# Kernel optimization log

Hardware: AMD Instinct MI355X
Metric: run time of the kernel (lower is better)

The kernel has to match this reference:

```python
import jax, jax.numpy as jnp
import numpy as np

B, LP, LQ, H = 16, 2048, 2048, 1024

def setup_inputs() -> dict:
    key = jax.random.key(0)
    k1, k2, k3 = jax.random.split(key, 3)
    proj_p = jax.random.normal(k1, (B, LP, H), dtype=jnp.float32)
    proj_q = jax.random.normal(k2, (B, LQ, H), dtype=jnp.float32)
    # nn.Linear(hidden_size, hidden_size): W stored as [out, in], y = x @ W.T + b
    W = jax.random.normal(k3, (H, H), dtype=jnp.float32) * (1.0 / np.sqrt(H))
    b = jnp.zeros((H,), dtype=jnp.float32)
    return {"proj_p": proj_p, "proj_q": proj_q, "W": W, "b": b}

def reference(proj_p, proj_q, W, b):
    # trans_q = Linear(proj_q)
    trans_q = jnp.einsum('bqh,oh->bqo', proj_q, W) + b            # [B,LQ,H]
    # UNscaled attention scores: proj_p @ trans_q^T
    att_weights = jnp.einsum('bph,bqh->bpq', proj_p, trans_q)     # [B,LP,LQ]
    att_norm = jax.nn.softmax(att_weights, axis=-1)
    att_vec = jnp.einsum('bpq,bqh->bph', att_norm, proj_q)        # [B,LP,H]
    # same linear weight reused, then ReLU
    out = jax.nn.relu(jnp.einsum('bph,oh->bpo', att_vec, W) + b)
    return out
```

## Files before the change

kernel.cpp:

```cpp
#include <hip/hip_runtime.h>

typedef _Float16 f16;
typedef _Float16 f16x8 __attribute__((ext_vector_type(8)));
typedef _Float16 f16x4 __attribute__((ext_vector_type(4)));
typedef float    f32x16 __attribute__((ext_vector_type(16)));

#define GLDS(gp, lp) __builtin_amdgcn_global_load_lds( \
    (const __attribute__((address_space(1))) void*)(gp), \
    (__attribute__((address_space(3))) void*)(lp), 16, 0, 0)

template<typename OUT_T, bool BIAS, bool RELU>
__global__ __launch_bounds__(256)
void gemm_bt(const f16* __restrict__ A, const f16* __restrict__ Bm,
             OUT_T* __restrict__ C, const float* __restrict__ bias,
             int M, int N, int K, long sA, long sB, long sC)
{
    __shared__ alignas(16) f16 As[128 * 32];
    __shared__ alignas(16) f16 Bs[128 * 32];

    int bx = blockIdx.x, by = blockIdx.y;
    {
        const int gx = gridDim.x;
        const int l = by * gx + bx;
        const int W = gx * 8;
        const int ygrp = l / W;
        const int rem = l - ygrp * W;
        bx = rem >> 3;
        by = ygrp * 8 + (rem & 7);
    }

    const int z = blockIdx.z;
    A  += (long)z * sA;
    Bm += (long)z * sB;
    C  += (long)z * sC;

    const int tid  = threadIdx.x;
    const int wid  = tid >> 6;
    const int lane = tid & 63;
    const int m0 = by * 128;
    const int n0 = bx * 128;
    const int wm = (wid >> 1) * 64;
    const int wn = (wid & 1) * 64;

    const int r0s  = tid >> 2;
    const int sgsw = ((tid & 3) ^ ((tid >> 3) & 3)) * 8;
    const f16* ag0 = A  + (long)(m0 + r0s) * K + sgsw;
    const f16* ag1 = A  + (long)(m0 + r0s + 64) * K + sgsw;
    const f16* bg0 = Bm + (long)(n0 + r0s) * K + sgsw;
    const f16* bg1 = Bm + (long)(n0 + r0s + 64) * K + sgsw;
    f16* asl0 = As + (wid * 64) * 8;
    f16* asl1 = As + (256 + wid * 64) * 8;
    f16* bsl0 = Bs + (wid * 64) * 8;
    f16* bsl1 = Bs + (256 + wid * 64) * 8;

    const int lr   = lane & 31;
    const int lh   = lane >> 5;
    const int swz  = (lr >> 1) & 3;
    const int off0 = ((lh ^ swz)) * 8;
    const int off1 = ((lh ^ swz) ^ 2) * 8;

    f32x16 acc[2][2];
#pragma unroll
    for (int i = 0; i < 2; ++i)
#pragma unroll
        for (int j = 0; j < 2; ++j)
#pragma unroll
            for (int r = 0; r < 16; ++r) acc[i][j][r] = 0.f;

    for (int kt = 0; kt < K; kt += 32) {
        GLDS(ag0 + kt, asl0);
        GLDS(ag1 + kt, asl1);
        GLDS(bg0 + kt, bsl0);
        GLDS(bg1 + kt, bsl1);
        __syncthreads();

        const f16* ar0 = As + (wm + lr) * 32;
        const f16* ar1 = As + (wm + 32 + lr) * 32;
        const f16* br0 = Bs + (wn + lr) * 32;
        const f16* br1 = Bs + (wn + 32 + lr) * 32;
        f16x8 af[2][2], bf[2][2];
        af[0][0] = *(const f16x8*)(ar0 + off0);
        af[0][1] = *(const f16x8*)(ar0 + off1);
        af[1][0] = *(const f16x8*)(ar1 + off0);
        af[1][1] = *(const f16x8*)(ar1 + off1);
        bf[0][0] = *(const f16x8*)(br0 + off0);
        bf[0][1] = *(const f16x8*)(br0 + off1);
        bf[1][0] = *(const f16x8*)(br1 + off0);
        bf[1][1] = *(const f16x8*)(br1 + off1);

#pragma unroll
        for (int ks = 0; ks < 2; ++ks)
#pragma unroll
            for (int mi = 0; mi < 2; ++mi)
#pragma unroll
                for (int ni = 0; ni < 2; ++ni)
                    acc[mi][ni] = __builtin_amdgcn_mfma_f32_32x32x16_f16(
                        af[mi][ks], bf[ni][ks], acc[mi][ni], 0, 0, 0);
        __syncthreads();
    }

    const int ec = lr;
#pragma unroll
    for (int ni = 0; ni < 2; ++ni) {
        const int gc = n0 + wn + ni * 32 + ec;
        const float bv = BIAS ? bias[gc] : 0.0f;
#pragma unroll
        for (int mi = 0; mi < 2; ++mi) {
#pragma unroll
            for (int r = 0; r < 16; ++r) {
                const int row = (r & 3) + 8 * (r >> 2) + 4 * lh;
                const int gr = m0 + wm + mi * 32 + row;
                float v = acc[mi][ni][r] + bv;
                if (RELU) v = fmaxf(v, 0.0f);
                C[(long)gr * N + gc] = (OUT_T)v;
            }
        }
    }
}

template<typename OUT_T, bool BIAS, bool RELU>
__global__ __launch_bounds__(512, 2)
void gemm_bt2(const f16* __restrict__ A, const f16* __restrict__ Bm,
              OUT_T* __restrict__ C, const float* __restrict__ bias,
              int M, int N, int K, long sA, long sB, long sC)
{
    constexpr int TSZ = 256 * 64;
    __shared__ alignas(16) f16 As[2 * TSZ];
    __shared__ alignas(16) f16 Bs[2 * TSZ];

    int bx = blockIdx.x, by = blockIdx.y;
    {
        const int gx = gridDim.x;
        const int l = by * gx + bx;
        const int W = gx * 8;
        const int ygrp = l / W;
        const int rem = l - ygrp * W;
        bx = rem >> 3;
        by = ygrp * 8 + (rem & 7);
    }
    const int z = blockIdx.z;
    A  += (long)z * sA;
    Bm += (long)z * sB;
    C  += (long)z * sC;

    const int tid  = threadIdx.x;
    const int wid  = tid >> 6;
    const int lane = tid & 63;
    const int lr = lane & 31;
    const int lh = lane >> 5;
    const int m0 = by * 256;
    const int n0 = bx * 256;
    const int wm = (wid >> 2) * 128;
    const int wn = (wid & 3) * 64;

    const int sr = tid >> 3;
    const int sg = ((tid & 7) ^ (sr & 7)) * 8;
    const f16* agS = A  + (long)(m0 + sr) * K + sg;
    const f16* bgS = Bm + (long)(n0 + sr) * K + sg;
    f16* aD = As + wid * (8 * 64);
    f16* bD = Bs + wid * (8 * 64);

    const int s7  = lr & 7;
    const int xs0 = ((0 + lh) ^ s7) * 8;
    const int xs1 = ((2 + lh) ^ s7) * 8;
    const int xs2 = ((4 + lh) ^ s7) * 8;
    const int xs3 = ((6 + lh) ^ s7) * 8;
    const f16* aR = As + (wm + lr) * 64;
    const f16* bR = Bs + (wn + lr) * 64;

    f32x16 acc[4][2];
#pragma unroll
    for (int mi = 0; mi < 4; ++mi)
#pragma unroll
        for (int ni = 0; ni < 2; ++ni)
#pragma unroll
            for (int r = 0; r < 16; ++r) acc[mi][ni][r] = 0.f;

    f16x8 b00, b01, b02, b03, b10, b11, b12, b13;

    const int NT = K >> 6;

#define GAc(buf, R0, kt) GLDS(agS + (long)(R0) * K + (kt), aD + (buf) * TSZ + (R0) * 64)
#define GBc(buf, R0, kt) GLDS(bgS + (long)(R0) * K + (kt), bD + (buf) * TSZ + (R0) * 64)

    GBc(0,   0, 0);  GBc(0,  64, 0);  GBc(0, 128, 0);  GBc(0, 192, 0);
    GAc(0,   0, 0);  GAc(0,  64, 0);  GAc(0, 128, 0);  GAc(0, 192, 0);
    GBc(1,   0, 64); GBc(1,  64, 64); GBc(1, 128, 64); GBc(1, 192, 64);
    GAc(1,   0, 64); GAc(1, 128, 64);
    asm volatile("s_waitcnt vmcnt(6)" ::: "memory");
    __builtin_amdgcn_s_barrier();

#define MFMA8(mi) \
    acc[mi][0] = __builtin_amdgcn_mfma_f32_32x32x16_f16(af0, b00, acc[mi][0], 0, 0, 0); \
    acc[mi][1] = __builtin_amdgcn_mfma_f32_32x32x16_f16(af0, b10, acc[mi][1], 0, 0, 0); \
    acc[mi][0] = __builtin_amdgcn_mfma_f32_32x32x16_f16(af1, b01, acc[mi][0], 0, 0, 0); \
    acc[mi][1] = __builtin_amdgcn_mfma_f32_32x32x16_f16(af1, b11, acc[mi][1], 0, 0, 0); \
    acc[mi][0] = __builtin_amdgcn_mfma_f32_32x32x16_f16(af2, b02, acc[mi][0], 0, 0, 0); \
    acc[mi][1] = __builtin_amdgcn_mfma_f32_32x32x16_f16(af2, b12, acc[mi][1], 0, 0, 0); \
    acc[mi][0] = __builtin_amdgcn_mfma_f32_32x32x16_f16(af3, b03, acc[mi][0], 0, 0, 0); \
    acc[mi][1] = __builtin_amdgcn_mfma_f32_32x32x16_f16(af3, b13, acc[mi][1], 0, 0, 0);

#define PH(buf, mi, VW, ...) { \
    if ((mi) == 0) { \
        b00 = *(const f16x8*)(bR + (buf) * TSZ + xs0); \
        b01 = *(const f16x8*)(bR + (buf) * TSZ + xs1); \
        b02 = *(const f16x8*)(bR + (buf) * TSZ + xs2); \
        b03 = *(const f16x8*)(bR + (buf) * TSZ + xs3); \
        b10 = *(const f16x8*)(bR + (buf) * TSZ + 2048 + xs0); \
        b11 = *(const f16x8*)(bR + (buf) * TSZ + 2048 + xs1); \
        b12 = *(const f16x8*)(bR + (buf) * TSZ + 2048 + xs2); \
        b13 = *(const f16x8*)(bR + (buf) * TSZ + 2048 + xs3); \
    } \
    f16x8 af0 = *(const f16x8*)(aR + (buf) * TSZ + (mi) * 2048 + xs0); \
    f16x8 af1 = *(const f16x8*)(aR + (buf) * TSZ + (mi) * 2048 + xs1); \
    f16x8 af2 = *(const f16x8*)(aR + (buf) * TSZ + (mi) * 2048 + xs2); \
    f16x8 af3 = *(const f16x8*)(aR + (buf) * TSZ + (mi) * 2048 + xs3); \
    __VA_ARGS__ \
    __builtin_amdgcn_s_barrier(); \
    asm volatile("s_waitcnt lgkmcnt(0)" ::: "memory"); \
    __builtin_amdgcn_s_setprio(1); \
    MFMA8(mi) \
    __builtin_amdgcn_s_setprio(0); \
    if (VW) { asm volatile("s_waitcnt vmcnt(6)" ::: "memory"); } \
    __builtin_amdgcn_s_barrier(); \
}

    for (int i = 0; i < NT / 2; ++i) {
        const long k1 = (long)(2 * i + 1) << 6;
        const long kA = (2 * i + 2 < NT) ? ((long)(2 * i + 2) << 6) : 0;
        const long kB = (2 * i + 3 < NT) ? ((long)(2 * i + 3) << 6) : 0;
        PH(0, 0, 0, GAc(1,  64, k1); GAc(1, 192, k1);)
        PH(0, 1, 0, GBc(0,   0, kA); GBc(0,  64, kA);)
        PH(0, 2, 0, GBc(0, 128, kA); GBc(0, 192, kA);)
        PH(0, 3, 1, GAc(0,   0, kA); GAc(0, 128, kA);)
        PH(1, 0, 0, GAc(0,  64, kA); GAc(0, 192, kA);)
        PH(1, 1, 0, GBc(1,   0, kB); GBc(1,  64, kB);)
        PH(1, 2, 0, GBc(1, 128, kB); GBc(1, 192, kB);)
        PH(1, 3, 1, GAc(1,   0, kB); GAc(1, 128, kB);)
    }

    asm volatile("s_waitcnt vmcnt(0)" ::: "memory");

#pragma unroll
    for (int ni = 0; ni < 2; ++ni) {
        const int gc = n0 + wn + ni * 32 + lr;
        const float bv = BIAS ? bias[gc] : 0.0f;
#pragma unroll
        for (int mi = 0; mi < 4; ++mi) {
#pragma unroll
            for (int r = 0; r < 16; ++r) {
                const int row = (r & 3) + 8 * (r >> 2) + 4 * lh;
                const int gr = m0 + wm + mi * 32 + row;
                float v = acc[mi][ni][r] + bv;
                if (RELU) v = fmaxf(v, 0.0f);
                C[(long)gr * N + gc] = (OUT_T)v;
            }
        }
    }
#undef PH
#undef MFMA8
#undef GAc
#undef GBc
}

__global__ __launch_bounds__(256)
void cast_f32_f16(const float* __restrict__ X, f16* __restrict__ Y)
{
    const long i = ((long)blockIdx.x * 256 + threadIdx.x) * 8;
    float4 a = *(const float4*)(X + i);
    float4 b = *(const float4*)(X + i + 4);
    f16x8 h = {(f16)a.x, (f16)a.y, (f16)a.z, (f16)a.w,
               (f16)b.x, (f16)b.y, (f16)b.z, (f16)b.w};
    *(f16x8*)(Y + i) = h;
}

__global__ __launch_bounds__(256)
void cast_q_dual(const float* __restrict__ X, f16* __restrict__ Yrow,
                 f16* __restrict__ Ytr)
{
    __shared__ f16 t[64][72];
    const float* Xb = X + (long)blockIdx.z * (2048L * 1024);
    f16* Yrb = Yrow + (long)blockIdx.z * (2048L * 1024);
    f16* Ytb = Ytr  + (long)blockIdx.z * (1024L * 2048);
    const int r0 = blockIdx.y * 64;
    const int c0 = blockIdx.x * 64;
    const int tid = threadIdx.x;
    const int tr = tid >> 4;
    const int tc = (tid & 15) * 4;
#pragma unroll
    for (int rr = 0; rr < 64; rr += 16) {
        float4 v = *(const float4*)(Xb + (long)(r0 + tr + rr) * 1024 + c0 + tc);
        f16x4 h = {(f16)v.x, (f16)v.y, (f16)v.z, (f16)v.w};
        *(f16x4*)&t[tr + rr][tc] = h;
        *(f16x4*)(Yrb + (long)(r0 + tr + rr) * 1024 + c0 + tc) = h;
    }
    __syncthreads();
#pragma unroll
    for (int rr = 0; rr < 64; rr += 16) {
        const int orow = tr + rr;
        f16x4 o = {t[tc + 0][orow], t[tc + 1][orow], t[tc + 2][orow], t[tc + 3][orow]};
        *(f16x4*)(Ytb + (long)(c0 + orow) * 2048 + r0 + tc) = o;
    }
}

__global__ __launch_bounds__(256)
void softmax_p(const float* __restrict__ S, f16* __restrict__ P)
{
    const long row = blockIdx.x;
    const float* s = S + row * 2048;
    f16* p = P + row * 2048;
    const int tid = threadIdx.x;
    const int wid = tid >> 6, lane = tid & 63;

    float4 a = *(const float4*)(s + tid * 8);
    float4 b = *(const float4*)(s + tid * 8 + 4);
    float v[8] = {a.x, a.y, a.z, a.w, b.x, b.y, b.z, b.w};

    float m = v[0];
#pragma unroll
    for (int j = 1; j < 8; ++j) m = fmaxf(m, v[j]);
#pragma unroll
    for (int off = 32; off > 0; off >>= 1) m = fmaxf(m, __shfl_xor(m, off, 64));

    __shared__ float red[8];
    if (lane == 0) red[wid] = m;
    __syncthreads();
    m = fmaxf(fmaxf(red[0], red[1]), fmaxf(red[2], red[3]));

    float sum = 0.f;
#pragma unroll
    for (int j = 0; j < 8; ++j) { v[j] = __expf(v[j] - m); sum += v[j]; }
#pragma unroll
    for (int off = 32; off > 0; off >>= 1) sum += __shfl_xor(sum, off, 64);
    if (lane == 0) red[4 + wid] = sum;
    __syncthreads();
    sum = red[4] + red[5] + red[6] + red[7];

    const float inv = 1.0f / sum;
    f16x8 h = {(f16)(v[0] * inv), (f16)(v[1] * inv), (f16)(v[2] * inv), (f16)(v[3] * inv),
               (f16)(v[4] * inv), (f16)(v[5] * inv), (f16)(v[6] * inv), (f16)(v[7] * inv)};
    *(f16x8*)(p + tid * 8) = h;
}

extern "C" void kernel_launch(void* const* d_in, const int* in_sizes, int n_in,
                              void* d_out, int out_size, void* d_ws, size_t ws_size,
                              hipStream_t stream)
{
    const float* proj_p = (const float*)d_in[0];
    const float* proj_q = (const float*)d_in[1];
    const float* W      = (const float*)d_in[2];
    const float* bias   = (const float*)d_in[3];
    float* out = (float*)d_out;

    constexpr long Bc = 16, L = 2048, H = 1024, NB = 4;
    constexpr long nPQ = Bc * L * H;

    char* ws = (char*)d_ws;
    f16*   pB  = (f16*)(ws + 0L);
    f16*   qB  = (f16*)(ws + 67108864L);
    f16*   qBt = (f16*)(ws + 134217728L);
    f16*   tQ  = (f16*)(ws + 201326592L);
    f16*   aV  = (f16*)(ws + 268435456L);
    f16*   Wb  = (f16*)(ws + 335544320L);
    float* S   = (float*)(ws + 337641472L);
    f16*   P   = (f16*)(ws + 404750336L);

    cast_f32_f16<<<nPQ / (256 * 8), 256, 0, stream>>>(proj_p, pB);
    cast_f32_f16<<<(H * H) / (256 * 8), 256, 0, stream>>>(W, Wb);
    cast_q_dual<<<dim3(16, 32, 16), 256, 0, stream>>>(proj_q, qB, qBt);

    gemm_bt2<f16, true, false><<<dim3(H / 256, (Bc * L) / 256, 1), 512, 0, stream>>>(
        qB, Wb, tQ, bias, (int)(Bc * L), (int)H, (int)H, 0, 0, 0);

    for (int c = 0; c < 4; ++c) {
        const long boff = (long)c * NB * L * H;
        gemm_bt2<float, false, false><<<dim3(L / 256, L / 256, NB), 512, 0, stream>>>(
            pB + boff, tQ + boff, S, nullptr, (int)L, (int)L, (int)H,
            L * H, L * H, L * L);
        softmax_p<<<NB * L, 256, 0, stream>>>(S, P);
        gemm_bt<f16, false, false><<<dim3(H / 128, L / 128, NB), 256, 0, stream>>>(
            P, qBt + (long)c * NB * H * L, aV + boff, nullptr, (int)L, (int)H, (int)L,
            L * L, H * L, L * H);
    }

    gemm_bt2<float, false, true><<<dim3(H / 256, (Bc * L) / 256, 1), 512, 0, stream>>>(
        aV, Wb, out, bias, (int)(Bc * L), (int)H, (int)H, 0, 0, 0);
}
```

Before: 994.7 us.

## Replace P·V GEMM with double-buffered 256x128 pipelined MFMA kernel

The attention-times-V GEMM moves from a simple 128x128, 256-thread kernel with a single LDS buffer and K-step 32 to a new 512-thread kernel with 256x128 tiles, K-step 64, double-buffered global-to-LDS loads interleaved with MFMA phases, XOR swizzling and setprio hints. The aim is to hide global load latency behind compute and raise operand reuse per tile. It costs more LDS per block and relies on hand-placed waitcnt and barrier ordering that must stay correct.

```diff
diff --git a/kernel.cpp b/kernel.cpp
--- a/kernel.cpp
+++ b/kernel.cpp
@@ -8,115 +8,6 @@
 #define GLDS(gp, lp) __builtin_amdgcn_global_load_lds( \
     (const __attribute__((address_space(1))) void*)(gp), \
     (__attribute__((address_space(3))) void*)(lp), 16, 0, 0)
-
-template<typename OUT_T, bool BIAS, bool RELU>
-__global__ __launch_bounds__(256)
-void gemm_bt(const f16* __restrict__ A, const f16* __restrict__ Bm,
-             OUT_T* __restrict__ C, const float* __restrict__ bias,
-             int M, int N, int K, long sA, long sB, long sC)
-{
-    __shared__ alignas(16) f16 As[128 * 32];
-    __shared__ alignas(16) f16 Bs[128 * 32];
-
-    int bx = blockIdx.x, by = blockIdx.y;
-    {
-        const int gx = gridDim.x;
-        const int l = by * gx + bx;
-        const int W = gx * 8;
-        const int ygrp = l / W;
-        const int rem = l - ygrp * W;
-        bx = rem >> 3;
-        by = ygrp * 8 + (rem & 7);
-    }
-
-    const int z = blockIdx.z;
-    A  += (long)z * sA;
-    Bm += (long)z * sB;
-    C  += (long)z * sC;
-
-    const int tid  = threadIdx.x;
-    const int wid  = tid >> 6;
-    const int lane = tid & 63;
-    const int m0 = by * 128;
-    const int n0 = bx * 128;
-    const int wm = (wid >> 1) * 64;
-    const int wn = (wid & 1) * 64;
-
-    const int r0s  = tid >> 2;
-    const int sgsw = ((tid & 3) ^ ((tid >> 3) & 3)) * 8;
-    const f16* ag0 = A  + (long)(m0 + r0s) * K + sgsw;
-    const f16* ag1 = A  + (long)(m0 + r0s + 64) * K + sgsw;
-    const f16* bg0 = Bm + (long)(n0 + r0s) * K + sgsw;
-    const f16* bg1 = Bm + (long)(n0 + r0s + 64) * K + sgsw;
-    f16* asl0 = As + (wid * 64) * 8;
-    f16* asl1 = As + (256 + wid * 64) * 8;
-    f16* bsl0 = Bs + (wid * 64) * 8;
-    f16* bsl1 = Bs + (256 + wid * 64) * 8;
-
-    const int lr   = lane & 31;
-    const int lh   = lane >> 5;
-    const int swz  = (lr >> 1) & 3;
-    const int off0 = ((lh ^ swz)) * 8;
-    const int off1 = ((lh ^ swz) ^ 2) * 8;
-
-    f32x16 acc[2][2];
-#pragma unroll
-    for (int i = 0; i < 2; ++i)
-#pragma unroll
-        for (int j = 0; j < 2; ++j)
-#pragma unroll
-            for (int r = 0; r < 16; ++r) acc[i][j][r] = 0.f;
-
-    for (int kt = 0; kt < K; kt += 32) {
-        GLDS(ag0 + kt, asl0);
-        GLDS(ag1 + kt, asl1);
-        GLDS(bg0 + kt, bsl0);
-        GLDS(bg1 + kt, bsl1);
-        __syncthreads();
-
-        const f16* ar0 = As + (wm + lr) * 32;
-        const f16* ar1 = As + (wm + 32 + lr) * 32;
-        const f16* br0 = Bs + (wn + lr) * 32;
-        const f16* br1 = Bs + (wn + 32 + lr) * 32;
-        f16x8 af[2][2], bf[2][2];
-        af[0][0] = *(const f16x8*)(ar0 + off0);
-        af[0][1] = *(const f16x8*)(ar0 + off1);
-        af[1][0] = *(const f16x8*)(ar1 + off0);
-        af[1][1] = *(const f16x8*)(ar1 + off1);
-        bf[0][0] = *(const f16x8*)(br0 + off0);
-        bf[0][1] = *(const f16x8*)(br0 + off1);
-        bf[1][0] = *(const f16x8*)(br1 + off0);
-        bf[1][1] = *(const f16x8*)(br1 + off1);
-
-#pragma unroll
-        for (int ks = 0; ks < 2; ++ks)
-#pragma unroll
-            for (int mi = 0; mi < 2; ++mi)
-#pragma unroll
-                for (int ni = 0; ni < 2; ++ni)
-                    acc[mi][ni] = __builtin_amdgcn_mfma_f32_32x32x16_f16(
-                        af[mi][ks], bf[ni][ks], acc[mi][ni], 0, 0, 0);
-        __syncthreads();
-    }
-
-    const int ec = lr;
-#pragma unroll
-    for (int ni = 0; ni < 2; ++ni) {
-        const int gc = n0 + wn + ni * 32 + ec;
-        const float bv = BIAS ? bias[gc] : 0.0f;
-#pragma unroll
-        for (int mi = 0; mi < 2; ++mi) {
-#pragma unroll
-            for (int r = 0; r < 16; ++r) {
-                const int row = (r & 3) + 8 * (r >> 2) + 4 * lh;
-                const int gr = m0 + wm + mi * 32 + row;
-                float v = acc[mi][ni][r] + bv;
-                if (RELU) v = fmaxf(v, 0.0f);
-                C[(long)gr * N + gc] = (OUT_T)v;
-            }
-        }
-    }
-}
 
 template<typename OUT_T, bool BIAS, bool RELU>
 __global__ __launch_bounds__(512, 2)
@@ -263,6 +154,147 @@
 #undef GBc
 }
 
+template<typename OUT_T, bool BIAS, bool RELU>
+__global__ __launch_bounds__(512, 2)
+void gemm_bt3(const f16* __restrict__ A, const f16* __restrict__ Bm,
+              OUT_T* __restrict__ C, const float* __restrict__ bias,
+              int M, int N, int K, long sA, long sB, long sC)
+{
+    constexpr int TSA = 256 * 64;
+    constexpr int TSB = 128 * 64;
+    __shared__ alignas(16) f16 As[2 * TSA];
+    __shared__ alignas(16) f16 Bs[2 * TSB];
+
+    int bx = blockIdx.x, by = blockIdx.y;
+    {
+        const int gx = gridDim.x;
+        const int l = by * gx + bx;
+        const int W = gx * 8;
+        const int ygrp = l / W;
+        const int rem = l - ygrp * W;
+        bx = rem >> 3;
+        by = ygrp * 8 + (rem & 7);
+    }
+    const int z = blockIdx.z;
+    A  += (long)z * sA;
+    Bm += (long)z * sB;
+    C  += (long)z * sC;
+
+    const int tid  = threadIdx.x;
+    const int wid  = tid >> 6;
+    const int lane = tid & 63;
+    const int lr = lane & 31;
+    const int lh = lane >> 5;
+    const int m0 = by * 256;
+    const int n0 = bx * 128;
+    const int wm = (wid >> 1) * 64;
+    const int wn = (wid & 1) * 64;
+
+    const int sr = tid >> 3;
+    const int sg = ((tid & 7) ^ (sr & 7)) * 8;
+    const f16* agS = A  + (long)(m0 + sr) * K + sg;
+    const f16* bgS = Bm + (long)(n0 + sr) * K + sg;
+    f16* aD = As + wid * (8 * 64);
+    f16* bD = Bs + wid * (8 * 64);
+
+    const int s7  = lr & 7;
+    const int xs0 = ((0 + lh) ^ s7) * 8;
+    const int xs1 = ((2 + lh) ^ s7) * 8;
+    const int xs2 = ((4 + lh) ^ s7) * 8;
+    const int xs3 = ((6 + lh) ^ s7) * 8;
+    const f16* aR = As + (wm + lr) * 64;
+    const f16* bR = Bs + (wn + lr) * 64;
+
+    f32x16 acc[2][2];
+#pragma unroll
+    for (int mi = 0; mi < 2; ++mi)
+#pragma unroll
+        for (int ni = 0; ni < 2; ++ni)
+#pragma unroll
+            for (int r = 0; r < 16; ++r) acc[mi][ni][r] = 0.f;
+
+    f16x8 b00, b01, b02, b03, b10, b11, b12, b13;
+
+    const int NT = K >> 6;
+
+#define GA3(buf, R0, kt) GLDS(agS + (long)(R0) * K + (kt), aD + (buf) * TSA + (R0) * 64)
+#define GB3(buf, R0, kt) GLDS(bgS + (long)(R0) * K + (kt), bD + (buf) * TSB + (R0) * 64)
+
+    GB3(0,   0, 0);  GB3(0,  64, 0);
+    GA3(0,   0, 0);  GA3(0,  64, 0);  GA3(0, 128, 0);  GA3(0, 192, 0);
+    GB3(1,   0, 64); GB3(1,  64, 64);
+    asm volatile("s_waitcnt vmcnt(2)" ::: "memory");
+    __builtin_amdgcn_s_barrier();
+
+#define MFMA8_3(mi) \
+    acc[mi][0] = __builtin_amdgcn_mfma_f32_32x32x16_f16(af0, b00, acc[mi][0], 0, 0, 0); \
+    acc[mi][1] = __builtin_amdgcn_mfma_f32_32x32x16_f16(af0, b10, acc[mi][1], 0, 0, 0); \
+    acc[mi][0] = __builtin_amdgcn_mfma_f32_32x32x16_f16(af1, b01, acc[mi][0], 0, 0, 0); \
+    acc[mi][1] = __builtin_amdgcn_mfma_f32_32x32x16_f16(af1, b11, acc[mi][1], 0, 0, 0); \
+    acc[mi][0] = __builtin_amdgcn_mfma_f32_32x32x16_f16(af2, b02, acc[mi][0], 0, 0, 0); \
+    acc[mi][1] = __builtin_amdgcn_mfma_f32_32x32x16_f16(af2, b12, acc[mi][1], 0, 0, 0); \
+    acc[mi][0] = __builtin_amdgcn_mfma_f32_32x32x16_f16(af3, b03, acc[mi][0], 0, 0, 0); \
+    acc[mi][1] = __builtin_amdgcn_mfma_f32_32x32x16_f16(af3, b13, acc[mi][1], 0, 0, 0);
+
+#define PH3(buf, mi, VW, ...) { \
+    if ((mi) == 0) { \
+        b00 = *(const f16x8*)(bR + (buf) * TSB + xs0); \
+        b01 = *(const f16x8*)(bR + (buf) * TSB + xs1); \
+        b02 = *(const f16x8*)(bR + (buf) * TSB + xs2); \
+        b03 = *(const f16x8*)(bR + (buf) * TSB + xs3); \
+        b10 = *(const f16x8*)(bR + (buf) * TSB + 2048 + xs0); \
+        b11 = *(const f16x8*)(bR + (buf) * TSB + 2048 + xs1); \
+        b12 = *(const f16x8*)(bR + (buf) * TSB + 2048 + xs2); \
+        b13 = *(const f16x8*)(bR + (buf) * TSB + 2048 + xs3); \
+    } \
+    f16x8 af0 = *(const f16x8*)(aR + (buf) * TSA + (mi) * 2048 + xs0); \
+    f16x8 af1 = *(const f16x8*)(aR + (buf) * TSA + (mi) * 2048 + xs1); \
+    f16x8 af2 = *(const f16x8*)(aR + (buf) * TSA + (mi) * 2048 + xs2); \
+    f16x8 af3 = *(const f16x8*)(aR + (buf) * TSA + (mi) * 2048 + xs3); \
+    __VA_ARGS__ \
+    __builtin_amdgcn_s_barrier(); \
+    asm volatile("s_waitcnt lgkmcnt(0)" ::: "memory"); \
+    __builtin_amdgcn_s_setprio(1); \
+    MFMA8_3(mi) \
+    __builtin_amdgcn_s_setprio(0); \
+    if (VW) { asm volatile("s_waitcnt vmcnt(2)" ::: "memory"); } \
+    __builtin_amdgcn_s_barrier(); \
+}
+
+    for (int i = 0; i < NT / 2; ++i) {
+        const long k1 = (long)(2 * i + 1) << 6;
+        const long kA = (2 * i + 2 < NT) ? ((long)(2 * i + 2) << 6) : 0;
+        const long kB = (2 * i + 3 < NT) ? ((long)(2 * i + 3) << 6) : 0;
+        PH3(0, 0, 0, GA3(1,   0, k1); GA3(1,  64, k1); GA3(1, 128, k1); GA3(1, 192, k1);)
+        PH3(0, 1, 1, GB3(0,   0, kA); GB3(0,  64, kA);)
+        PH3(1, 0, 0, GA3(0,   0, kA); GA3(0,  64, kA); GA3(0, 128, kA); GA3(0, 192, kA);)
+        PH3(1, 1, 1, GB3(1,   0, kB); GB3(1,  64, kB);)
+    }
+
+    asm volatile("s_waitcnt vmcnt(0)" ::: "memory");
+
+#pragma unroll
+    for (int ni = 0; ni < 2; ++ni) {
+        const int gc = n0 + wn + ni * 32 + lr;
+        const float bv = BIAS ? bias[gc] : 0.0f;
+#pragma unroll
+        for (int mi = 0; mi < 2; ++mi) {
+#pragma unroll
+            for (int r = 0; r < 16; ++r) {
+                const int row = (r & 3) + 8 * (r >> 2) + 4 * lh;
+                const int gr = m0 + wm + mi * 32 + row;
+                float v = acc[mi][ni][r] + bv;
+                if (RELU) v = fmaxf(v, 0.0f);
+                C[(long)gr * N + gc] = (OUT_T)v;
+            }
+        }
+    }
+#undef PH3
+#undef MFMA8_3
+#undef GA3
+#undef GB3
+}
+
 __global__ __launch_bounds__(256)
 void cast_f32_f16(const float* __restrict__ X, f16* __restrict__ Y)
 {
@@ -378,7 +410,7 @@
             pB + boff, tQ + boff, S, nullptr, (int)L, (int)L, (int)H,
             L * H, L * H, L * L);
         softmax_p<<<NB * L, 256, 0, stream>>>(S, P);
-        gemm_bt<f16, false, false><<<dim3(H / 128, L / 128, NB), 256, 0, stream>>>(
+        gemm_bt3<f16, false, false><<<dim3(H / 128, L / 256, NB), 512, 0, stream>>>(
             P, qBt + (long)c * NB * H * L, aV + boff, nullptr, (int)L, (int)H, (int)L,
             L * L, H * L, L * H);
     }
```

Result: faster. 968.3 us (-2.7%).
